# Kernel tuning notes

Hardware: AMD Instinct MI355X
Metric: run time of the kernel (lower is better)

Reference implementation:

```python
import jax, jax.numpy as jnp
import numpy as np

NEG_INF = -1.0e9  # masked_fill value used by the torch module
LN_EPS = 1e-6


def setup_inputs() -> dict:
    key = jax.random.key(0)
    ks = jax.random.split(key, 10)
    B, S, D = 4, 1024, 1024
    H, DK, DV = 16, 64, 64
    q = jax.random.normal(ks[0], (B, S, D), dtype=jnp.float32)
    k = jax.random.normal(ks[1], (B, S, D), dtype=jnp.float32)
    v = jax.random.normal(ks[2], (B, S, D), dtype=jnp.float32)
    mask = jax.random.randint(ks[3], (B, S, S), 0, 2, dtype=jnp.int32)
    sc = 1.0 / np.sqrt(D)
    wq = jax.random.normal(ks[4], (H, D, DK), dtype=jnp.float32) * sc  # per-head W_qs stacked
    wk = jax.random.normal(ks[5], (H, D, DK), dtype=jnp.float32) * sc
    wv = jax.random.normal(ks[6], (H, D, DV), dtype=jnp.float32) * sc
    fc_w = jax.random.normal(ks[7], (D, H * DV), dtype=jnp.float32) * (1.0 / np.sqrt(H * DV))  # torch Linear weight [out,in]
    ln_g = jnp.ones((D,), dtype=jnp.float32)
    ln_b = jnp.zeros((D,), dtype=jnp.float32)
    return {"q": q, "k": k, "v": v, "mask": mask, "wq": wq, "wk": wk,
            "wv": wv, "fc_w": fc_w, "ln_g": ln_g, "ln_b": ln_b}


def reference(q, k, v, mask, wq, wk, wv, fc_w, ln_g, ln_b):
    # Batched equivalent of the per-head Python loop (dropout in eval mode = identity).
    B, S, D = q.shape
    H, _, DK = wq.shape
    DV = wv.shape[-1]
    temperature = jnp.asarray(DK, q.dtype) ** 0.5
    residual = q
    qh = jnp.einsum('bqd,hdk->bhqk', q, wq)   # [B,H,Q,DK]
    kh = jnp.einsum('bsd,hdk->bhsk', k, wk)   # [B,H,K,DK]
    vh = jnp.einsum('bsd,hdv->bhsv', v, wv)   # [B,H,K,DV]
    attn = jnp.einsum('bhqe,bhke->bhqk', qh / temperature, kh)  # [B,H,Q,K]
    attn = jnp.where(mask[:, None, :, :] == 0, jnp.asarray(NEG_INF, attn.dtype), attn)
    attn = jax.nn.softmax(attn, axis=-1)
    heads = jnp.einsum('bhqk,bhkv->bhqv', attn, vh)             # [B,H,Q,DV]
    # concat heads along feature dim in head order (matches torch.cat of the loop outputs)
    concat = jnp.transpose(heads, (0, 2, 1, 3)).reshape(B, S, H * DV)
    out = concat @ fc_w.T                                        # fc, no bias
    out = out + residual
    mu = jnp.mean(out, axis=-1, keepdims=True)
    var = jnp.mean(jnp.square(out - mu), axis=-1, keepdims=True)
    out = (out - mu) / jnp.sqrt(var + LN_EPS) * ln_g + ln_b
    return out
```

## Files before the change

### kernel.cpp

```cpp
#include <hip/hip_runtime.h>
#include <hip/hip_bf16.h>

typedef __bf16 bf16x8 __attribute__((ext_vector_type(8)));
typedef __bf16 bf16x4 __attribute__((ext_vector_type(4)));
typedef __bf16 bf16x2 __attribute__((ext_vector_type(2)));
typedef float f32x4 __attribute__((ext_vector_type(4)));
typedef unsigned int u32x2 __attribute__((ext_vector_type(2)));

#define MFMA16(a, b, c) __builtin_amdgcn_mfma_f32_16x16x32_bf16(a, b, c, 0, 0, 0)

static constexpr int M_ = 4096;

__device__ __forceinline__ void gload_lds16(const void* g, void* l) {
  __builtin_amdgcn_global_load_lds((const __attribute__((address_space(1))) void*)g,
                                   (__attribute__((address_space(3))) void*)l, 16, 0, 0);
}

__device__ __forceinline__ float exp2_hw(float x) {
  float r;
  asm("v_exp_f32 %0, %1" : "=v"(r) : "v"(x));
  return r;
}

__device__ __forceinline__ bf16x8 cvt8(float4 x, float4 y) {
  bf16x8 o;
  o[0] = (__bf16)x.x; o[1] = (__bf16)x.y; o[2] = (__bf16)x.z; o[3] = (__bf16)x.w;
  o[4] = (__bf16)y.x; o[5] = (__bf16)y.y; o[6] = (__bf16)y.z; o[7] = (__bf16)y.w;
  return o;
}

#define SWZ(rowv, c16) (((rowv) * 64) + (((c16) ^ ((rowv) & 7)) * 8))

__global__ __launch_bounds__(256) void prep(const float* __restrict__ fc_w,
                                            const float* __restrict__ wq,
                                            const float* __restrict__ wk,
                                            const float* __restrict__ wv,
                                            const int* __restrict__ mask,
                                            __bf16* __restrict__ WFC,
                                            __bf16* __restrict__ W3T,
                                            unsigned long long* __restrict__ bits) {
  __shared__ float tile[64][65];
  int bx = blockIdx.x;
  const int t = threadIdx.x;

  if (bx < 512) {
    int i = bx * 256 + t;
    const float4* p = (const float4*)fc_w + (size_t)i * 2;
    float4 a = p[0], b = p[1];
    *((bf16x8*)WFC + i) = cvt8(a, b);
    return;
  }
  bx -= 512;
  if (bx < 768) {
    const int z = bx >> 8, rem = bx & 255;
    const float* w = z == 0 ? wq : (z == 1 ? wk : wv);
    const float scale = z == 0 ? 0.125f * 1.4426950408889634f : 1.0f;
    __bf16* o = W3T + (size_t)z * 1048576;
    const int h = rem & 15, d0 = (rem >> 4) * 64;
    const int r = t >> 2, c0 = (t & 3) * 16;
    const float4* s4 = (const float4*)(w + ((size_t)h * 1024 + d0 + r) * 64 + c0);
#pragma unroll
    for (int j = 0; j < 4; ++j) {
      float4 vv = s4[j];
      tile[r][c0 + 4 * j + 0] = vv.x; tile[r][c0 + 4 * j + 1] = vv.y;
      tile[r][c0 + 4 * j + 2] = vv.z; tile[r][c0 + 4 * j + 3] = vv.w;
    }
    __syncthreads();
    __bf16* dst = o + ((size_t)(h * 64 + r)) * 1024 + d0 + c0;
    bf16x8 o0, o1;
#pragma unroll
    for (int j = 0; j < 8; ++j) o0[j] = (__bf16)(tile[c0 + j][r] * scale);
#pragma unroll
    for (int j = 0; j < 8; ++j) o1[j] = (__bf16)(tile[c0 + 8 + j][r] * scale);
    *(bf16x8*)dst = o0;
    *(bf16x8*)(dst + 8) = o1;
    return;
  }
  bx -= 768;
  {
    const int wid = bx * 4 + (t >> 6);
    const int lane = t & 63;
#pragma unroll
    for (int i = 0; i < 16; ++i) {
      int widx = wid * 16 + i;
      int qrow = widx & 1023;
      int bkt = widx >> 10;
      int b = bkt >> 4, kt = bkt & 15;
      int mval = mask[((size_t)b * 1024 + qrow) * 1024 + kt * 64 + lane];
      unsigned long long bal = __ballot(mval != 0);
      if (lane == 0) bits[widx] = bal;
    }
  }
}

__global__ __launch_bounds__(256) void gemm_qkv(const float* __restrict__ q,
                                                const float* __restrict__ k,
                                                const float* __restrict__ v,
                                                const __bf16* __restrict__ Btbase,
                                                __bf16* __restrict__ HEADS) {
  __shared__ __bf16 SMEM[24576];
  const int L = blockIdx.x;
  const int wl = (L & 7) * 96 + (L >> 3);
  const int bn = wl & 7;
  const int bmz = wl >> 3;
  const int bm = bmz & 31, z = bmz >> 5;
  const float* Af = z == 0 ? q : (z == 1 ? k : v);
  const __bf16* Bt = Btbase + (size_t)z * 1048576;
  const int tid = threadIdx.x, lane = tid & 63;
  const int w = tid >> 6;
  const int wr = (w >> 1) * 64, wc = (w & 1) * 64;
  const int lr = lane & 15, lh = lane >> 4;
  const int t16 = tid * 16;
  char* smem = (char*)SMEM;

  const char* apA = (const char*)Af +
                    ((size_t)(bm * 128 + (tid >> 3)) * 4096) +
                    (((tid & 7) ^ ((tid >> 3) & 7)) * 16);
  const char* apB = (const char*)Bt +
                    ((size_t)(bn * 128 + (tid >> 2)) * 2048) +
                    (((tid & 3) ^ ((tid >> 2) & 3)) * 16);

#define QSTAGE(buf)                                              \
  do {                                                           \
    char* da = smem + (buf) * 16384;                             \
    gload_lds16(apA, da + t16);                                  \
    gload_lds16(apA + 131072, da + 4096 + t16);                  \
    gload_lds16(apA + 262144, da + 8192 + t16);                  \
    gload_lds16(apA + 393216, da + 12288 + t16);                 \
    char* db = smem + 32768 + (buf) * 8192;                      \
    gload_lds16(apB, db + t16);                                  \
    gload_lds16(apB + 131072, db + 4096 + t16);                  \
    apA += 128; apB += 64;                                       \
  } while (0)

  const int aswz0 = (((2 * lh) ^ (lr & 7)) * 16);
  const int aswz1 = (((2 * lh + 1) ^ (lr & 7)) * 16);
  const int bswz = ((lh ^ (lr & 3)) * 16);

  f32x4 acc[4][4];
#pragma unroll
  for (int m = 0; m < 4; ++m)
#pragma unroll
    for (int n = 0; n < 4; ++n) {
      f32x4 zz = {0.f, 0.f, 0.f, 0.f};
      acc[m][n] = zz;
    }

  QSTAGE(0);
  __syncthreads();

  for (int kt = 0; kt < 32; ++kt) {
    const int cur = kt & 1;
    if (kt < 31) QSTAGE(cur ^ 1);
    const int abase = cur * 16384;
    const int bbase = 32768 + cur * 8192;
    bf16x8 af[4], bfr[4];
#pragma unroll
    for (int m = 0; m < 4; ++m) {
      const char* ap = smem + abase + (wr + m * 16 + lr) * 128;
      float4 f0 = *(const float4*)(ap + aswz0);
      float4 f1 = *(const float4*)(ap + aswz1);
      af[m] = cvt8(f0, f1);
    }
#pragma unroll
    for (int n = 0; n < 4; ++n)
      bfr[n] = *(const bf16x8*)(smem + bbase + (wc + n * 16 + lr) * 64 + bswz);
    __builtin_amdgcn_s_setprio(1);
#pragma unroll
    for (int m = 0; m < 4; ++m)
#pragma unroll
      for (int n = 0; n < 4; ++n) acc[m][n] = MFMA16(af[m], bfr[n], acc[m][n]);
    __builtin_amdgcn_s_setprio(0);
    __syncthreads();
  }
#undef QSTAGE

  if (z == 2) {
    const int hl = w & 1;
    const size_t vtbase = 2ull * 4194304;
    const size_t bb2 = (size_t)(bm >> 3) * 16 + bn * 2;
    const int kkbase = (bm & 7) * 128;
#pragma unroll
    for (int p = 0; p < 2; ++p) {
      if (hl == p) {
#pragma unroll
        for (int m = 0; m < 4; ++m)
#pragma unroll
          for (int n = 0; n < 4; ++n) {
            const int dk = n * 16 + lr;
            const int s = wr + m * 16 + lh * 4;
            bf16x4 pv;
#pragma unroll
            for (int j = 0; j < 4; ++j) pv[j] = (__bf16)acc[m][n][j];
            *(bf16x4*)&SMEM[dk * 132 + s] = pv;
          }
      }
      __syncthreads();
      {
        const int dk = tid >> 2, sc = tid & 3;
        const __bf16* srcp = &SMEM[dk * 132 + sc * 32];
        __bf16* dstp = HEADS + vtbase + ((bb2 + p) * 64 + dk) * 1024 + kkbase + sc * 32;
#pragma unroll
        for (int u = 0; u < 8; ++u) *(bf16x4*)(dstp + u * 4) = *(const bf16x4*)(srcp + u * 4);
      }
      __syncthreads();
    }
    return;
  }

#pragma unroll
  for (int p = 0; p < 2; ++p) {
    if ((w >> 1) == p) {
#pragma unroll
      for (int m = 0; m < 4; ++m)
#pragma unroll
        for (int n = 0; n < 4; ++n)
#pragma unroll
          for (int reg = 0; reg < 4; ++reg)
            SMEM[(m * 16 + lh * 4 + reg) * 132 + wc + n * 16 + lr] = (__bf16)acc[m][n][reg];
    }
    __syncthreads();
    {
      const int rowl = tid >> 2, c0 = (tid & 3) * 32;
      const int row = bm * 128 + p * 64 + rowl;
      const int b = row >> 10, s = row & 1023;
      const int h = bn * 2 + (c0 >> 6), dk0 = c0 & 63;
      __bf16* dst = HEADS + (size_t)z * 4194304 + (((size_t)b * 16 + h) * 1024 + s) * 64 + dk0;
      const __bf16* srcp = &SMEM[rowl * 132 + c0];
#pragma unroll
      for (int u = 0; u < 8; ++u) *(bf16x4*)(dst + u * 4) = *(const bf16x4*)(srcp + u * 4);
    }
    __syncthreads();
  }
}

__global__ __launch_bounds__(256) void gemm_fc64(const __bf16* __restrict__ A,
                                                 const __bf16* __restrict__ Bt,
                                                 float* __restrict__ O,
                                                 const float* __restrict__ resid) {
  __shared__ __bf16 SMEM[12288];
  const int L = blockIdx.x;
  const int wl = (L & 7) * 64 + (L >> 3);
  const int bn = wl & 7, bm = wl >> 3;
  const int tid = threadIdx.x, lane = tid & 63;
  const int w = tid >> 6;
  const int wc = w * 32;
  const int lr = lane & 15, lh = lane >> 4;

  const int o0 = tid * 16;
  const int row0 = o0 >> 6, cb = o0 & 63;
  const char* apA = (const char*)A + ((size_t)(bm * 64 + row0) * 1024) * 2 + cb;
  const char* apB0 = (const char*)Bt + ((size_t)(bn * 128 + row0) * 1024) * 2 + cb;
  const char* apB1 = apB0 + 64 * 2048;
  char* smem = (char*)SMEM;

#define FSTAGE(buf)                                         \
  do {                                                      \
    gload_lds16(apA, smem + (buf) * 4096 + o0);             \
    char* dd = smem + 8192 + (buf) * 8192;                  \
    gload_lds16(apB0, dd + o0);                             \
    gload_lds16(apB1, dd + 4096 + o0);                      \
    apA += 64; apB0 += 64; apB1 += 64;                      \
  } while (0)

  f32x4 acc[4][2];
#pragma unroll
  for (int m = 0; m < 4; ++m)
#pragma unroll
    for (int n = 0; n < 2; ++n) {
      f32x4 z = {0.f, 0.f, 0.f, 0.f};
      acc[m][n] = z;
    }

  FSTAGE(0);
  __syncthreads();

  for (int kt = 0; kt < 32; ++kt) {
    const int cur = kt & 1;
    if (kt < 31) FSTAGE(cur ^ 1);
    const int ab = cur * 2048;
    const int bb = 4096 + cur * 4096;
    bf16x8 af[4], bfr[2];
#pragma unroll
    for (int m = 0; m < 4; ++m) af[m] = *(const bf16x8*)&SMEM[ab + (m * 16 + lr) * 32 + lh * 8];
#pragma unroll
    for (int n = 0; n < 2; ++n)
      bfr[n] = *(const bf16x8*)&SMEM[bb + (wc + n * 16 + lr) * 32 + lh * 8];
    __builtin_amdgcn_s_setprio(1);
#pragma unroll
    for (int m = 0; m < 4; ++m)
#pragma unroll
      for (int n = 0; n < 2; ++n) acc[m][n] = MFMA16(af[m], bfr[n], acc[m][n]);
    __builtin_amdgcn_s_setprio(0);
    __syncthreads();
  }
#undef FSTAGE

#pragma unroll
  for (int m = 0; m < 4; ++m)
#pragma unroll
    for (int n = 0; n < 2; ++n)
#pragma unroll
      for (int reg = 0; reg < 4; ++reg) {
        int row = bm * 64 + m * 16 + lh * 4 + reg;
        int col = bn * 128 + wc + n * 16 + lr;
        size_t idx = (size_t)row * 1024 + col;
        O[idx] = acc[m][n][reg] + resid[idx];
      }
}

__global__ __launch_bounds__(256, 4) void attn_kernel(const __bf16* __restrict__ HEADS,
                                                      const unsigned long long* __restrict__ m64,
                                                      __bf16* __restrict__ concat) {
  const __bf16* QH = HEADS;
  const __bf16* KH = HEADS + (size_t)M_ * 1024;
  const __bf16* VT = HEADS + (size_t)2 * M_ * 1024;
  __shared__ __bf16 Ks[2][2][32 * 64];
  __shared__ __bf16 Vs[2][2][64 * 32];
  __shared__ unsigned Psw[2][4][256];

  const int d = blockIdx.x;
  const int xcd = d & 7, j = d >> 3;
  const int grp = xcd * 8 + (j >> 4);
  const int qt = j & 15;
  const int h = grp & 15, b = grp >> 4;

  const int tid = threadIdx.x, lane = tid & 63, w = tid >> 6;
  const int lr = lane & 15, lh = lane >> 4;
  const size_t headoff = ((size_t)b * 16 + h) * 65536;
  const char* Kbase = (const char*)(KH + headoff);
  const char* Vbase = (const char*)(VT + headoff);

  const int krow = tid >> 3, kg = tid & 7;
  const int kgo = krow * 128 + ((kg ^ (krow & 7)) * 16);
  const int vrow = tid >> 2, vg = tid & 3;
  const int vgo = vrow * 2048 + ((vg ^ ((vrow >> 1) & 3)) * 16);
  const int ldsb = tid * 16;

  const char* kpA = Kbase + kgo;
  const char* kpB = Kbase + 65536 + kgo;
  const char* vpA = Vbase + vgo;
  const char* vpB = Vbase + 1024 + vgo;

#define STAGE(buf)                                          \
  do {                                                      \
    gload_lds16(kpA, (char*)Ks[buf][0] + ldsb);             \
    gload_lds16(kpB, (char*)Ks[buf][1] + ldsb);             \
    gload_lds16(vpA, (char*)Vs[buf][0] + ldsb);             \
    gload_lds16(vpB, (char*)Vs[buf][1] + ldsb);             \
    kpA += 4096; kpB += 4096; vpA += 64; vpB += 64;         \
  } while (0)

  const int qrow = qt * 64 + w * 16 + lr;
  bf16x8 qa[2];
  {
    const __bf16* qptr = QH + headoff + (size_t)qrow * 64 + lh * 8;
    qa[0] = *(const bf16x8*)qptr;
    qa[1] = *(const bf16x8*)(qptr + 32);
  }
  f32x4 oacc[4];
#pragma unroll
  for (int g = 0; g < 4; ++g) {
    f32x4 z = {0.f, 0.f, 0.f, 0.f};
    oacc[g] = z;
  }
  float lrun = 0.f;

  const unsigned long long* m64A = m64 + (size_t)b * 16384 + qrow;
  const unsigned long long* m64B = m64A + 8192;
  unsigned long long pairA = m64A[0], pairB = m64B[0];
  unsigned long long pairAn = 0, pairBn = 0;

  const int vcol = (lh ^ ((lr >> 1) & 3)) * 8;
  const int pread = lr * 32 + vcol;
  const int pG = (lr >> 1) & 3;
  int kread[2][2], vread[4];
#pragma unroll
  for (int n = 0; n < 2; ++n)
#pragma unroll
    for (int h2 = 0; h2 < 2; ++h2) kread[n][h2] = SWZ(n * 16 + lr, h2 * 4 + lh);
#pragma unroll
  for (int g = 0; g < 4; ++g) vread[g] = (g * 16 + lr) * 32 + vcol;

  STAGE(0);
  __syncthreads();

#pragma unroll 2
  for (int t = 0; t < 16; ++t) {
    const int cur = t & 1;
    if ((t & 1) == 0 && t < 14) {
      pairAn = m64A[((t >> 1) + 1) * 1024];
      pairBn = m64B[((t >> 1) + 1) * 1024];
    }
    const unsigned mwA = (t & 1) ? (unsigned)(pairA >> 32) : (unsigned)pairA;
    const unsigned mwB = (t & 1) ? (unsigned)(pairB >> 32) : (unsigned)pairB;
    if (t < 15) STAGE(cur ^ 1);

    f32x4 sA[2], sB[2];
#pragma unroll
    for (int n = 0; n < 2; ++n) {
      f32x4 z = {0.f, 0.f, 0.f, 0.f};
      sA[n] = z; sB[n] = z;
    }
    __builtin_amdgcn_s_setprio(1);
#pragma unroll
    for (int n = 0; n < 2; ++n)
#pragma unroll
      for (int h2 = 0; h2 < 2; ++h2) {
        bf16x8 kbA = *(const bf16x8*)&Ks[cur][0][kread[n][h2]];
        bf16x8 kbB = *(const bf16x8*)&Ks[cur][1][kread[n][h2]];
        sA[n] = MFMA16(kbA, qa[h2], sA[n]);
        sB[n] = MFMA16(kbB, qa[h2], sB[n]);
      }
    __builtin_amdgcn_s_setprio(0);

#pragma unroll
    for (int n = 0; n < 2; ++n)
#pragma unroll
      for (int r = 0; r < 4; ++r) {
        unsigned bit = (mwA >> (n * 16 + lh * 4 + r)) & 1u;
        float p = bit ? exp2_hw(sA[n][r]) : 0.0f;
        sA[n][r] = p;
        lrun += p;
      }
#pragma unroll
    for (int n = 0; n < 2; ++n)
#pragma unroll
      for (int r = 0; r < 4; ++r) {
        unsigned bit = (mwB >> (n * 16 + lh * 4 + r)) & 1u;
        float p = bit ? exp2_hw(sB[n][r]) : 0.0f;
        sB[n][r] = p;
        lrun += p;
      }

#pragma unroll
    for (int n = 0; n < 2; ++n) {
      bf16x2 p0, p1;
      p0[0] = (__bf16)sA[n][0]; p0[1] = (__bf16)sA[n][1];
      p1[0] = (__bf16)sA[n][2]; p1[1] = (__bf16)sA[n][3];
      int G = n * 2 + (lh >> 1);
      int addr = lr * 16 + ((G ^ pG) * 4) + (lh & 1) * 2;
      u32x2 wv;
      wv[0] = __builtin_bit_cast(unsigned, p0);
      wv[1] = __builtin_bit_cast(unsigned, p1);
      *(u32x2*)&Psw[0][w][addr] = wv;
    }
#pragma unroll
    for (int n = 0; n < 2; ++n) {
      bf16x2 p0, p1;
      p0[0] = (__bf16)sB[n][0]; p0[1] = (__bf16)sB[n][1];
      p1[0] = (__bf16)sB[n][2]; p1[1] = (__bf16)sB[n][3];
      int G = n * 2 + (lh >> 1);
      int addr = lr * 16 + ((G ^ pG) * 4) + (lh & 1) * 2;
      u32x2 wv;
      wv[0] = __builtin_bit_cast(unsigned, p0);
      wv[1] = __builtin_bit_cast(unsigned, p1);
      *(u32x2*)&Psw[1][w][addr] = wv;
    }
    bf16x8 paA = *(const bf16x8*)&((const __bf16*)Psw[0][w])[pread];
    bf16x8 paB = *(const bf16x8*)&((const __bf16*)Psw[1][w])[pread];

    __builtin_amdgcn_s_setprio(1);
#pragma unroll
    for (int g = 0; g < 4; ++g) {
      bf16x8 vbA = *(const bf16x8*)&Vs[cur][0][vread[g]];
      bf16x8 vbB = *(const bf16x8*)&Vs[cur][1][vread[g]];
      oacc[g] = MFMA16(paA, vbA, oacc[g]);
      oacc[g] = MFMA16(paB, vbB, oacc[g]);
    }
    __builtin_amdgcn_s_setprio(0);
    if (t & 1) { pairA = pairAn; pairB = pairBn; }
    __syncthreads();
  }
#undef STAGE

  lrun += __shfl_xor(lrun, 16, 64);
  lrun += __shfl_xor(lrun, 32, 64);
  const float linv = 1.0f / (lrun + 1e-30f);
  const int qg0 = qt * 64 + w * 16 + lh * 4;
#pragma unroll
  for (int r = 0; r < 4; ++r) {
    const float ir = __shfl(linv, (lane & 48) | (lh * 4 + r), 64);
#pragma unroll
    for (int g = 0; g < 4; ++g)
      concat[((size_t)b * 1024 + qg0 + r) * 1024 + h * 64 + g * 16 + lr] =
          (__bf16)(oacc[g][r] * ir);
  }
}

__global__ __launch_bounds__(256) void ln_kernel(const float* __restrict__ in,
                                                 const float* __restrict__ gam,
                                                 const float* __restrict__ bet,
                                                 float* __restrict__ out) {
  const int row = blockIdx.x, t = threadIdx.x;
  const float4* x4 = (const float4*)(in + (size_t)row * 1024);
  float4 v = x4[t];
  float s = v.x + v.y + v.z + v.w;
  float sq = v.x * v.x + v.y * v.y + v.z * v.z + v.w * v.w;
#pragma unroll
  for (int off = 1; off < 64; off <<= 1) {
    s += __shfl_xor(s, off, 64);
    sq += __shfl_xor(sq, off, 64);
  }
  __shared__ float red[8];
  const int w = t >> 6, lane = t & 63;
  if (lane == 0) { red[w] = s; red[4 + w] = sq; }
  __syncthreads();
  s = red[0] + red[1] + red[2] + red[3];
  sq = red[4] + red[5] + red[6] + red[7];
  const float mu = s * (1.0f / 1024.0f);
  const float var = sq * (1.0f / 1024.0f) - mu * mu;
  const float rstd = rsqrtf(var + 1e-6f);
  float4 g4 = ((const float4*)gam)[t];
  float4 b4 = ((const float4*)bet)[t];
  float4 o;
  o.x = (v.x - mu) * rstd * g4.x + b4.x;
  o.y = (v.y - mu) * rstd * g4.y + b4.y;
  o.z = (v.z - mu) * rstd * g4.z + b4.z;
  o.w = (v.w - mu) * rstd * g4.w + b4.w;
  ((float4*)(out + (size_t)row * 1024))[t] = o;
}

extern "C" void kernel_launch(void* const* d_in, const int* in_sizes, int n_in,
                              void* d_out, int out_size, void* d_ws, size_t ws_size,
                              hipStream_t stream) {
  (void)in_sizes; (void)n_in; (void)out_size; (void)ws_size;
  const float* q = (const float*)d_in[0];
  const float* k = (const float*)d_in[1];
  const float* v = (const float*)d_in[2];
  const int* mask = (const int*)d_in[3];
  const float* wq = (const float*)d_in[4];
  const float* wk = (const float*)d_in[5];
  const float* wv = (const float*)d_in[6];
  const float* fc_w = (const float*)d_in[7];
  const float* ln_g = (const float*)d_in[8];
  const float* ln_b = (const float*)d_in[9];
  float* out = (float*)d_out;

  __bf16* QKVBF = (__bf16*)d_ws;
  __bf16* W3T   = QKVBF + 3ull * 4194304;
  __bf16* WFC   = W3T + 3ull * 1048576;
  __bf16* HEADS = WFC + 1048576;
  __bf16* CONCAT = HEADS + 3ull * 4194304;
  float* OUT1 = (float*)(CONCAT + 4194304);
  unsigned long long* MASKB = (unsigned long long*)OUT1;

  prep<<<2304, 256, 0, stream>>>(fc_w, wq, wk, wv, mask, WFC, W3T, MASKB);
  gemm_qkv<<<768, 256, 0, stream>>>(q, k, v, W3T, HEADS);
  attn_kernel<<<1024, 256, 0, stream>>>(HEADS, MASKB, CONCAT);
  gemm_fc64<<<512, 256, 0, stream>>>(CONCAT, WFC, OUT1, q);
  ln_kernel<<<4096, 256, 0, stream>>>(OUT1, ln_g, ln_b, out);
}
```

Measured before the change: 115.3 us.

## Register-prefetch fp32 A tile, convert to bf16 before LDS, double K step

The QKV projection GEMM now loads the fp32 activation tile into registers, converts it to bf16 once, and stores it to a single-buffered swizzled LDS tile. This replaces async global-to-LDS fp32 copies that every wave converted separately. The K step per iteration doubles from 32 to 64, which halves the number of loop iterations and barriers, and launch bounds now request 3 blocks per CU. In exchange, each iteration adds a second barrier, the A loads go through registers instead of direct-to-LDS, and register pressure rises with the 8 float4 prefetch buffers.

Result: slower. 141.9 us (+23.0%).

```diff
diff --git a/kernel.cpp b/kernel.cpp
--- a/kernel.cpp
+++ b/kernel.cpp
@@ -93,11 +93,11 @@
   }
 }
 
-__global__ __launch_bounds__(256) void gemm_qkv(const float* __restrict__ q,
-                                                const float* __restrict__ k,
-                                                const float* __restrict__ v,
-                                                const __bf16* __restrict__ Btbase,
-                                                __bf16* __restrict__ HEADS) {
+__global__ __launch_bounds__(256, 3) void gemm_qkv(const float* __restrict__ q,
+                                                   const float* __restrict__ k,
+                                                   const float* __restrict__ v,
+                                                   const __bf16* __restrict__ Btbase,
+                                                   __bf16* __restrict__ HEADS) {
   __shared__ __bf16 SMEM[24576];
   const int L = blockIdx.x;
   const int wl = (L & 7) * 96 + (L >> 3);
@@ -110,32 +110,37 @@
   const int w = tid >> 6;
   const int wr = (w >> 1) * 64, wc = (w & 1) * 64;
   const int lr = lane & 15, lh = lane >> 4;
+  char* smem = (char*)SMEM;
   const int t16 = tid * 16;
-  char* smem = (char*)SMEM;
-
-  const char* apA = (const char*)Af +
-                    ((size_t)(bm * 128 + (tid >> 3)) * 4096) +
+
+  const int rA = tid >> 1;
+  const float* apA = Af + (size_t)(bm * 128 + rA) * 1024 + (tid & 1) * 32;
+  int awr[4];
+#pragma unroll
+  for (int j = 0; j < 4; ++j)
+    awr[j] = rA * 128 + ((((tid & 1) * 4 + j) ^ (rA & 7)) * 16);
+
+  const char* apB = (const char*)Bt + ((size_t)(bn * 128 + (tid >> 3)) * 2048) +
                     (((tid & 7) ^ ((tid >> 3) & 7)) * 16);
-  const char* apB = (const char*)Bt +
-                    ((size_t)(bn * 128 + (tid >> 2)) * 2048) +
-                    (((tid & 3) ^ ((tid >> 2) & 3)) * 16);
-
-#define QSTAGE(buf)                                              \
-  do {                                                           \
-    char* da = smem + (buf) * 16384;                             \
-    gload_lds16(apA, da + t16);                                  \
-    gload_lds16(apA + 131072, da + 4096 + t16);                  \
-    gload_lds16(apA + 262144, da + 8192 + t16);                  \
-    gload_lds16(apA + 393216, da + 12288 + t16);                 \
-    char* db = smem + 32768 + (buf) * 8192;                      \
-    gload_lds16(apB, db + t16);                                  \
-    gload_lds16(apB + 131072, db + 4096 + t16);                  \
-    apA += 128; apB += 64;                                       \
+
+#define BSTAGE(buf)                                          \
+  do {                                                       \
+    char* db = smem + 16384 + (buf) * 16384;                 \
+    gload_lds16(apB, db + t16);                              \
+    gload_lds16(apB + 65536, db + 4096 + t16);               \
+    gload_lds16(apB + 131072, db + 8192 + t16);              \
+    gload_lds16(apB + 196608, db + 12288 + t16);             \
+    apB += 128;                                              \
   } while (0)
 
-  const int aswz0 = (((2 * lh) ^ (lr & 7)) * 16);
-  const int aswz1 = (((2 * lh + 1) ^ (lr & 7)) * 16);
-  const int bswz = ((lh ^ (lr & 3)) * 16);
+  int ard[4][2], brd[4][2];
+#pragma unroll
+  for (int m = 0; m < 4; ++m)
+#pragma unroll
+    for (int ks = 0; ks < 2; ++ks) {
+      ard[m][ks] = (wr + m * 16 + lr) * 128 + (((ks * 4 + lh) ^ (lr & 7)) * 16);
+      brd[m][ks] = (wc + m * 16 + lr) * 128 + (((ks * 4 + lh) ^ (lr & 7)) * 16);
+    }
 
   f32x4 acc[4][4];
 #pragma unroll
@@ -146,34 +151,50 @@
       acc[m][n] = zz;
     }
 
-  QSTAGE(0);
+  {
+    float4 a[8];
+#pragma unroll
+    for (int j = 0; j < 8; ++j) a[j] = *(const float4*)(apA + j * 4);
+#pragma unroll
+    for (int j = 0; j < 4; ++j)
+      *(bf16x8*)(smem + awr[j]) = cvt8(a[2 * j], a[2 * j + 1]);
+  }
+  BSTAGE(0);
   __syncthreads();
 
-  for (int kt = 0; kt < 32; ++kt) {
+  for (int kt = 0; kt < 16; ++kt) {
     const int cur = kt & 1;
-    if (kt < 31) QSTAGE(cur ^ 1);
-    const int abase = cur * 16384;
-    const int bbase = 32768 + cur * 8192;
-    bf16x8 af[4], bfr[4];
-#pragma unroll
-    for (int m = 0; m < 4; ++m) {
-      const char* ap = smem + abase + (wr + m * 16 + lr) * 128;
-      float4 f0 = *(const float4*)(ap + aswz0);
-      float4 f1 = *(const float4*)(ap + aswz1);
-      af[m] = cvt8(f0, f1);
-    }
-#pragma unroll
-    for (int n = 0; n < 4; ++n)
-      bfr[n] = *(const bf16x8*)(smem + bbase + (wc + n * 16 + lr) * 64 + bswz);
-    __builtin_amdgcn_s_setprio(1);
-#pragma unroll
-    for (int m = 0; m < 4; ++m)
-#pragma unroll
-      for (int n = 0; n < 4; ++n) acc[m][n] = MFMA16(af[m], bfr[n], acc[m][n]);
-    __builtin_amdgcn_s_setprio(0);
-    __syncthreads();
-  }
-#undef QSTAGE
+    float4 a[8];
+    if (kt < 15) {
+      const float* pa = apA + (size_t)(kt + 1) * 64;
+#pragma unroll
+      for (int j = 0; j < 8; ++j) a[j] = *(const float4*)(pa + j * 4);
+      BSTAGE(cur ^ 1);
+    }
+    const int bbase = 16384 + cur * 16384;
+#pragma unroll
+    for (int ks = 0; ks < 2; ++ks) {
+      bf16x8 af[4], bfr[4];
+#pragma unroll
+      for (int m = 0; m < 4; ++m) af[m] = *(const bf16x8*)(smem + ard[m][ks]);
+#pragma unroll
+      for (int n = 0; n < 4; ++n) bfr[n] = *(const bf16x8*)(smem + bbase + brd[n][ks]);
+      __builtin_amdgcn_s_setprio(1);
+#pragma unroll
+      for (int m = 0; m < 4; ++m)
+#pragma unroll
+        for (int n = 0; n < 4; ++n) acc[m][n] = MFMA16(af[m], bfr[n], acc[m][n]);
+      __builtin_amdgcn_s_setprio(0);
+    }
+    __syncthreads();
+    if (kt < 15) {
+#pragma unroll
+      for (int j = 0; j < 4; ++j)
+        *(bf16x8*)(smem + awr[j]) = cvt8(a[2 * j], a[2 * j + 1]);
+    }
+    __syncthreads();
+  }
+#undef BSTAGE
 
   if (z == 2) {
     const int hl = w & 1;
```
